# Optimization experiments

Measured on AMD Instinct MI355X. Metric: run time of the kernel, lower is better.

The kernel has to match this reference:

```python
import jax, jax.numpy as jnp
import numpy as np

B, C_IN, C_QKV, N = 8, 12, 36, 4096

def setup_inputs() -> dict:
    key = jax.random.key(0)
    ks = jax.random.split(key, 9)
    s_in = 1.0 / np.sqrt(C_IN)
    s_o = 1.0 / np.sqrt(C_QKV)
    return {
        "x": jax.random.normal(ks[0], (B, C_IN, N), dtype=jnp.float32),
        "wq": jax.random.uniform(ks[1], (C_QKV, C_IN), jnp.float32, -s_in, s_in),
        "bq": jax.random.uniform(ks[2], (C_QKV,), jnp.float32, -s_in, s_in),
        "wk": jax.random.uniform(ks[3], (C_QKV, C_IN), jnp.float32, -s_in, s_in),
        "bk": jax.random.uniform(ks[4], (C_QKV,), jnp.float32, -s_in, s_in),
        "wv": jax.random.uniform(ks[5], (C_QKV, C_IN), jnp.float32, -s_in, s_in),
        "bv": jax.random.uniform(ks[6], (C_QKV,), jnp.float32, -s_in, s_in),
        "wo": jax.random.uniform(ks[7], (C_IN, C_QKV), jnp.float32, -s_o, s_o),
        "bo": jax.random.uniform(ks[8], (C_IN,), jnp.float32, -s_o, s_o),
    }

def _conv1x1(w, b, x):
    # 1x1 Conv1d == channel-mixing matmul: [o,i] @ [b,i,n] -> [b,o,n]
    return jnp.einsum('oi,bin->bon', w, x) + b[None, :, None]

def reference(x, wq, bq, wk, bk, wv, bv, wo, bo):
    scale = 1.0 / jnp.sqrt(jnp.float32(x.shape[1]))  # 1/sqrt(12)
    q = _conv1x1(wq, bq, x)  # [B, 36, N]
    k = _conv1x1(wk, bk, x)
    v = _conv1x1(wv, bv, x)
    # inter = k^T @ q : scores[b,n,m] = sum_c k[b,c,n] * q[b,c,m]
    scores = jnp.einsum('bcn,bcm->bnm', k, q) * scale  # [B, N, N]
    weights = jax.nn.softmax(scores, axis=-1)
    attn = jnp.einsum('bcn,bnm->bcm', v, weights)  # v @ weights, [B, 36, N]
    return _conv1x1(wo, bo, attn)  # [B, 12, N]
```

## Files before the change

kernel.cpp:

```cpp
#include <hip/hip_runtime.h>
#include <hip/hip_bf16.h>
#include <math.h>

#define B 8
#define CIN 12
#define CQ 36
#define CP 48
#define N 4096
#define SCALE 0.28867513459481287f
#define LOG2E 1.4426950408889634f
#define ZSPLIT 8
#define NCHUNK (N / ZSPLIT)
#define NT (NCHUNK / 32)
#define MSPLIT 4

typedef __attribute__((ext_vector_type(4)))  short bf4_t;
typedef __attribute__((ext_vector_type(8)))  short bf8_t;
typedef __attribute__((ext_vector_type(16))) float f32x16;
typedef __attribute__((ext_vector_type(4)))  float f32x4;

__device__ __forceinline__ unsigned short f2bf(float x) {
  unsigned int u = __float_as_uint(x);
  u += 0x7FFFu + ((u >> 16) & 1u);
  return (unsigned short)(u >> 16);
}

#if __has_builtin(__builtin_amdgcn_cvt_pk_bf16_f32)
typedef __attribute__((ext_vector_type(2))) __bf16 bf16x2_t;
__device__ __forceinline__ unsigned pk2bf(float a, float b) {
  bf16x2_t v = __builtin_amdgcn_cvt_pk_bf16_f32(a, b);
  return __builtin_bit_cast(unsigned, v);
}
#else
__device__ __forceinline__ unsigned pk2bf(float a, float b) {
  return (__float_as_uint(a) >> 16) | (__float_as_uint(b) & 0xFFFF0000u);
}
#endif

__device__ __forceinline__ float bf2f(unsigned short u) {
  return __uint_as_float((unsigned)u << 16);
}

__device__ __forceinline__ float exp2fast(float x) {
#if __has_builtin(__builtin_amdgcn_exp2f)
  return __builtin_amdgcn_exp2f(x);
#else
  return exp2f(x);
#endif
}

__device__ __forceinline__ f32x4 mfma16(bf4_t a, bf4_t b, f32x4 c) {
#if __has_builtin(__builtin_amdgcn_mfma_f32_16x16x16bf16_1k)
  return __builtin_amdgcn_mfma_f32_16x16x16bf16_1k(a, b, c, 0, 0, 0);
#else
  bf8_t a8 = {a[0], a[1], a[2], a[3], 0, 0, 0, 0};
  bf8_t b8 = {b[0], b[1], b[2], b[3], 0, 0, 0, 0};
  return __builtin_amdgcn_mfma_f32_16x16x32_bf16(a8, b8, c, 0, 0, 0);
#endif
}

__device__ __forceinline__ bf8_t lds_bf8(const unsigned short* p) {
  uint2 a = *(const uint2*)p;
  uint2 b = *(const uint2*)(p + 4);
  uint4 r{a.x, a.y, b.x, b.y};
  return __builtin_bit_cast(bf8_t, r);
}
__device__ __forceinline__ void wlds16(unsigned short* p, uint4 v) {
  *(uint2*)p = uint2{v.x, v.y};
  *(uint2*)(p + 4) = uint2{v.z, v.w};
}

__global__ __launch_bounds__(256) void qkv_kernel(
    const float* __restrict__ x,
    const float* __restrict__ wq, const float* __restrict__ bq,
    const float* __restrict__ wk, const float* __restrict__ bk,
    const float* __restrict__ wv, const float* __restrict__ bv,
    unsigned short* __restrict__ qT, unsigned short* __restrict__ kT,
    unsigned short* __restrict__ vbf) {
  __shared__ float sw[CQ * CIN];
  __shared__ float sb[CQ];
  int z = blockIdx.y;
  const float* w  = (z == 0) ? wq : (z == 1) ? wk : wv;
  const float* bb = (z == 0) ? bq : (z == 1) ? bk : bv;
  float scale = (z == 1) ? SCALE * LOG2E : 1.0f;
  int tid = threadIdx.x;
  for (int e = tid; e < CQ * CIN; e += 256) sw[e] = w[e] * scale;
  if (tid < CQ) sb[tid] = bb[tid] * scale;
  __syncthreads();
  int gid = blockIdx.x * 256 + tid;
  int b = gid >> 12;
  int n = gid & (N - 1);
  float xv[CIN];
#pragma unroll
  for (int i = 0; i < CIN; ++i) xv[i] = x[(b * CIN + i) * N + n];
  if (z == 2) {
#pragma unroll
    for (int o = 0; o < CQ; ++o) {
      float a = sb[o];
#pragma unroll
      for (int i = 0; i < CIN; ++i) a += sw[o * CIN + i] * xv[i];
      vbf[((size_t)b * CP + o) * N + n] = f2bf(a);
    }
  } else {
    __attribute__((aligned(16))) unsigned row[CP / 2];
#pragma unroll
    for (int o = 0; o < CQ; o += 2) {
      float a0 = sb[o], a1 = sb[o + 1];
#pragma unroll
      for (int i = 0; i < CIN; ++i) {
        float xi = xv[i];
        a0 += sw[o * CIN + i] * xi;
        a1 += sw[(o + 1) * CIN + i] * xi;
      }
      row[o / 2] = (unsigned)f2bf(a0) | ((unsigned)f2bf(a1) << 16);
    }
    row[18] = (z == 0) ? 0x3F803F80u : 0u;
#pragma unroll
    for (int o = 19; o < CP / 2; ++o) row[o] = 0;
    unsigned short* dst = ((z == 0) ? qT : kT) + ((size_t)b * N + n) * CP;
#pragma unroll
    for (int i = 0; i < 6; ++i) *(uint4*)(dst + 8 * i) = *(const uint4*)&row[4 * i];
  }
}

__global__ __launch_bounds__(256) void stats_kernel(
    const unsigned short* __restrict__ qT, const unsigned short* __restrict__ kT,
    float* __restrict__ psum) {
  __shared__ float red[4][32];
  int tid = threadIdx.x, lane = tid & 63, wave = tid >> 6;
  int b = blockIdx.y, nblk = blockIdx.x, ms = blockIdx.z;
  int l31 = lane & 31, h = lane >> 5;
  const unsigned short* krow = kT + ((size_t)b * N + nblk * 32 + l31) * CP + h * 8;
  bf8_t a0 = *(const bf8_t*)(krow);
  bf8_t a1 = *(const bf8_t*)(krow + 16);
  bf8_t a2 = *(const bf8_t*)(krow + 32);
  float rs[16];
#pragma unroll
  for (int r = 0; r < 16; ++r) rs[r] = 0.f;
  const int MW = N / MSPLIT / 4;
  const unsigned short* qbase =
      qT + ((size_t)b * N + ms * (N / MSPLIT) + wave * MW + l31) * CP + h * 8;
#pragma unroll 2
  for (int t = 0; t < MW / 32; ++t) {
    const unsigned short* qrow2 = qbase + (size_t)t * 32 * CP;
    bf8_t b0 = *(const bf8_t*)(qrow2);
    bf8_t b1 = *(const bf8_t*)(qrow2 + 16);
    bf8_t b2 = *(const bf8_t*)(qrow2 + 32);
    f32x16 S;
#pragma unroll
    for (int r = 0; r < 16; ++r) S[r] = 0.f;
    S = __builtin_amdgcn_mfma_f32_32x32x16_bf16(a0, b0, S, 0, 0, 0);
    S = __builtin_amdgcn_mfma_f32_32x32x16_bf16(a1, b1, S, 0, 0, 0);
    S = __builtin_amdgcn_mfma_f32_32x32x16_bf16(a2, b2, S, 0, 0, 0);
#pragma unroll
    for (int r = 0; r < 16; ++r) rs[r] += exp2fast(S[r]);
  }
#pragma unroll
  for (int off = 16; off >= 1; off >>= 1)
#pragma unroll
    for (int r = 0; r < 16; ++r) rs[r] += __shfl_xor(rs[r], off, 32);
  if (l31 == 0) {
#pragma unroll
    for (int r = 0; r < 16; ++r) {
      int row = (r & 3) + 8 * (r >> 2) + 4 * h;
      red[wave][row] = rs[r];
    }
  }
  __syncthreads();
  if (tid < 32) {
    float s = red[0][tid] + red[1][tid] + red[2][tid] + red[3][tid];
    psum[((size_t)ms * B + b) * N + nblk * 32 + tid] = s;
  }
}

__global__ __launch_bounds__(256) void finalize_kernel(
    const float* __restrict__ psum, unsigned short* __restrict__ kT) {
  int gid = blockIdx.x * 256 + threadIdx.x;
  float L = 0.f;
#pragma unroll
  for (int ms = 0; ms < MSPLIT; ++ms) L += psum[(size_t)ms * B * N + gid];
  float t = -__log2f(L);
  unsigned short hi = f2bf(t);
  unsigned short lo = f2bf(t - bf2f(hi));
  size_t base = (size_t)gid * CP;
  kT[base + 36] = hi;
  kT[base + 37] = lo;
}

__global__ __launch_bounds__(256) void init_kernel(
    float* __restrict__ out, const float* __restrict__ bo) {
  int gid = blockIdx.x * 256 + threadIdx.x;
  int e4 = gid * 4;
  int i = (e4 >> 12) % CIN;
  float bv = bo[i];
  *(float4*)(out + e4) = float4{bv, bv, bv, bv};
}

__global__ __launch_bounds__(256, 5) void attn_kernel(
    const unsigned short* __restrict__ qT, const unsigned short* __restrict__ kT,
    const unsigned short* __restrict__ vbf, const float* __restrict__ wo,
    float* __restrict__ out) {
  __shared__ unsigned short kbuf[2][32 * 52];
  __shared__ unsigned short vbuf[2][48 * 36];
  __shared__ unsigned short plds[4][32 * 40];
  int tid = threadIdx.x, lane = tid & 63, wave = tid >> 6;
  int b = blockIdx.y, z = blockIdx.z, mblk = blockIdx.x;
  int l31 = lane & 31, h = lane >> 5, l15 = lane & 15, q4 = lane >> 4;
  int m0 = mblk * 128 + wave * 32;
  size_t bN = (size_t)b * N;
  bool isK0 = tid < 192;
  int r0row = isK0 ? (tid / 6) : ((tid - 192) >> 2);
  int r0c   = isK0 ? (tid % 6) : ((tid - 192) & 3);
  const unsigned short* s0 = isK0
      ? kT + (bN + z * NCHUNK + r0row) * CP + r0c * 8
      : vbf + ((size_t)b * CP + r0row) * N + z * NCHUNK + r0c * 8;
  int s0stride = isK0 ? 32 * CP : 32;
  unsigned short* dst0 = isK0 ? &kbuf[0][r0row * 52 + r0c * 8]
                              : &vbuf[0][r0row * 36 + r0c * 8];
  int dbs0 = isK0 ? 32 * 52 : 48 * 36;
  bool has1 = tid < 128;
  int r1row = (tid >> 2) + 16;
  int r1c = tid & 3;
  const unsigned short* s1 =
      vbf + ((size_t)b * CP + r1row) * N + z * NCHUNK + r1c * 8;
  unsigned short* dst1 = &vbuf[0][r1row * 36 + r1c * 8];
  const int dbs1 = 48 * 36;
  const unsigned short* qrow = qT + (bN + m0 + l31) * CP + h * 8;
  bf8_t qb0 = *(const bf8_t*)(qrow);
  bf8_t qb1 = *(const bf8_t*)(qrow + 16);
  bf8_t qb2 = *(const bf8_t*)(qrow + 32);
  bf4_t woa[3];
#pragma unroll
  for (int ct = 0; ct < 3; ++ct) {
    float4 w4 = {0.f, 0.f, 0.f, 0.f};
    int col = 16 * ct + q4 * 4;
    if (l15 < CIN && col < CQ) w4 = *(const float4*)(wo + l15 * CQ + col);
    woa[ct] = bf4_t{(short)f2bf(w4.x), (short)f2bf(w4.y),
                    (short)f2bf(w4.z), (short)f2bf(w4.w)};
  }
  f32x4 acc[3][2];
#pragma unroll
  for (int ct = 0; ct < 3; ++ct)
#pragma unroll
    for (int hm = 0; hm < 2; ++hm)
#pragma unroll
      for (int r = 0; r < 4; ++r) acc[ct][hm][r] = 0.f;
  unsigned short* pl = plds[wave];
  uint4 r0 = *(const uint4*)s0; s0 += s0stride;
  uint4 r1{0, 0, 0, 0};
  if (has1) { r1 = *(const uint4*)s1; s1 += 32; }
  wlds16(dst0, r0);
  if (has1) wlds16(dst1, r1);
  __syncthreads();
  for (int t = 0; t < NT; ++t) {
    int buf = t & 1;
    if (t + 1 < NT) {
      r0 = *(const uint4*)s0; s0 += s0stride;
      if (has1) { r1 = *(const uint4*)s1; s1 += 32; }
    }
    const unsigned short* kb = kbuf[buf];
    const unsigned short* vb = vbuf[buf];
    bf8_t a0 = lds_bf8(kb + l31 * 52 + h * 8);
    bf8_t a1 = lds_bf8(kb + l31 * 52 + h * 8 + 16);
    bf8_t a2 = lds_bf8(kb + l31 * 52 + h * 8 + 32);
    f32x16 S;
#pragma unroll
    for (int r = 0; r < 16; ++r) S[r] = 0.f;
    S = __builtin_amdgcn_mfma_f32_32x32x16_bf16(a0, qb0, S, 0, 0, 0);
    S = __builtin_amdgcn_mfma_f32_32x32x16_bf16(a1, qb1, S, 0, 0, 0);
    S = __builtin_amdgcn_mfma_f32_32x32x16_bf16(a2, qb2, S, 0, 0, 0);
#pragma unroll
    for (int qd = 0; qd < 4; ++qd) {
      uint2 pk;
      pk.x = pk2bf(exp2fast(S[4 * qd + 0]), exp2fast(S[4 * qd + 1]));
      pk.y = pk2bf(exp2fast(S[4 * qd + 2]), exp2fast(S[4 * qd + 3]));
      *(uint2*)&pl[l31 * 40 + 8 * qd + 4 * h] = pk;
    }
    bf8_t pb0 = *(const bf8_t*)&pl[l15 * 40 + q4 * 8];
    bf8_t pb1 = *(const bf8_t*)&pl[(16 + l15) * 40 + q4 * 8];
    bf8_t v0 = lds_bf8(vb + (0 * 16 + l15) * 36 + q4 * 8);
    bf8_t v1 = lds_bf8(vb + (1 * 16 + l15) * 36 + q4 * 8);
    bf8_t v2 = lds_bf8(vb + (2 * 16 + l15) * 36 + q4 * 8);
    acc[0][0] = __builtin_amdgcn_mfma_f32_16x16x32_bf16(v0, pb0, acc[0][0], 0, 0, 0);
    acc[0][1] = __builtin_amdgcn_mfma_f32_16x16x32_bf16(v0, pb1, acc[0][1], 0, 0, 0);
    acc[1][0] = __builtin_amdgcn_mfma_f32_16x16x32_bf16(v1, pb0, acc[1][0], 0, 0, 0);
    acc[1][1] = __builtin_amdgcn_mfma_f32_16x16x32_bf16(v1, pb1, acc[1][1], 0, 0, 0);
    acc[2][0] = __builtin_amdgcn_mfma_f32_16x16x32_bf16(v2, pb0, acc[2][0], 0, 0, 0);
    acc[2][1] = __builtin_amdgcn_mfma_f32_16x16x32_bf16(v2, pb1, acc[2][1], 0, 0, 0);
    if (t + 1 < NT) {
      int nb = buf ^ 1;
      wlds16(dst0 + nb * dbs0, r0);
      if (has1) wlds16(dst1 + nb * dbs1, r1);
    }
    __syncthreads();
  }
#pragma unroll
  for (int hm = 0; hm < 2; ++hm) {
    f32x4 po = {0.f, 0.f, 0.f, 0.f};
#pragma unroll
    for (int ct = 0; ct < 3; ++ct) {
      union { uint2 u; bf4_t v; } pb;
      pb.u.x = pk2bf(acc[ct][hm][0], acc[ct][hm][1]);
      pb.u.y = pk2bf(acc[ct][hm][2], acc[ct][hm][3]);
      po = mfma16(woa[ct], pb.v, po);
    }
    if (q4 < 3) {
      float* ob = out + ((size_t)b * CIN + q4 * 4) * N + m0 + hm * 16 + l15;
#pragma unroll
      for (int r = 0; r < 4; ++r) atomicAdd(ob + (size_t)r * N, po[r]);
    }
  }
}

extern "C" void kernel_launch(void* const* d_in, const int* in_sizes, int n_in,
                              void* d_out, int out_size, void* d_ws, size_t ws_size,
                              hipStream_t stream) {
  const float* x  = (const float*)d_in[0];
  const float* wq = (const float*)d_in[1];
  const float* bq = (const float*)d_in[2];
  const float* wk = (const float*)d_in[3];
  const float* bk = (const float*)d_in[4];
  const float* wv = (const float*)d_in[5];
  const float* bv = (const float*)d_in[6];
  const float* wo = (const float*)d_in[7];
  const float* bo = (const float*)d_in[8];
  float* out = (float*)d_out;

  char* ws = (char*)d_ws;
  unsigned short* qT  = (unsigned short*)ws;
  unsigned short* kT  = (unsigned short*)(ws + 3145728);
  unsigned short* vbf = (unsigned short*)(ws + 2 * 3145728);
  float* psum = (float*)(ws + 3 * 3145728);

  qkv_kernel<<<dim3(B * N / 256, 3), 256, 0, stream>>>(x, wq, bq, wk, bk, wv, bv,
                                                       qT, kT, vbf);
  stats_kernel<<<dim3(N / 32, B, MSPLIT), 256, 0, stream>>>(qT, kT, psum);
  finalize_kernel<<<B * N / 256, 256, 0, stream>>>(psum, kT);
  init_kernel<<<B * CIN * N / 1024, 256, 0, stream>>>(out, bo);
  attn_kernel<<<dim3(N / 128, B, ZSPLIT), 256, 0, stream>>>(qT, kT, vbf, wo, out);
}
```

Measured before the change: 151.4 us.

## Double per-wave tile in stats and attention kernels, merge finalize and init

The stats kernel now handles 64 key rows per block, with two accumulators sharing each loaded q fragment, and MSPLIT drops to 2. The attention kernel gives each wave 64 query columns instead of 32, so every K/V tile staged in LDS is reused twice and global traffic per unit of work halves. The finalize and init kernels are merged into one prep kernel, saving a launch. In exchange, register use and LDS per block go up, launch bounds fall from 5 to 3 blocks, and the grids shrink, which may leave parts of the GPU idle.

```diff
diff --git a/kernel.cpp b/kernel.cpp
--- a/kernel.cpp
+++ b/kernel.cpp
@@ -12,7 +12,7 @@
 #define ZSPLIT 8
 #define NCHUNK (N / ZSPLIT)
 #define NT (NCHUNK / 32)
-#define MSPLIT 4
+#define MSPLIT 2
 
 typedef __attribute__((ext_vector_type(4)))  short bf4_t;
 typedef __attribute__((ext_vector_type(8)))  short bf8_t;
@@ -126,87 +126,104 @@
 __global__ __launch_bounds__(256) void stats_kernel(
     const unsigned short* __restrict__ qT, const unsigned short* __restrict__ kT,
     float* __restrict__ psum) {
-  __shared__ float red[4][32];
+  __shared__ float red[4][64];
   int tid = threadIdx.x, lane = tid & 63, wave = tid >> 6;
   int b = blockIdx.y, nblk = blockIdx.x, ms = blockIdx.z;
   int l31 = lane & 31, h = lane >> 5;
-  const unsigned short* krow = kT + ((size_t)b * N + nblk * 32 + l31) * CP + h * 8;
-  bf8_t a0 = *(const bf8_t*)(krow);
-  bf8_t a1 = *(const bf8_t*)(krow + 16);
-  bf8_t a2 = *(const bf8_t*)(krow + 32);
-  float rs[16];
-#pragma unroll
-  for (int r = 0; r < 16; ++r) rs[r] = 0.f;
+  int n0 = nblk * 64;
+  size_t bN = (size_t)b * N;
+  const unsigned short* krow0 = kT + (bN + n0 + l31) * CP + h * 8;
+  const unsigned short* krow1 = krow0 + (size_t)32 * CP;
+  bf8_t a0 = *(const bf8_t*)(krow0);
+  bf8_t a1 = *(const bf8_t*)(krow0 + 16);
+  bf8_t a2 = *(const bf8_t*)(krow0 + 32);
+  bf8_t a3 = *(const bf8_t*)(krow1);
+  bf8_t a4 = *(const bf8_t*)(krow1 + 16);
+  bf8_t a5 = *(const bf8_t*)(krow1 + 32);
+  float rs0[16], rs1[16];
+#pragma unroll
+  for (int r = 0; r < 16; ++r) { rs0[r] = 0.f; rs1[r] = 0.f; }
   const int MW = N / MSPLIT / 4;
   const unsigned short* qbase =
-      qT + ((size_t)b * N + ms * (N / MSPLIT) + wave * MW + l31) * CP + h * 8;
+      qT + (bN + ms * (N / MSPLIT) + wave * MW + l31) * CP + h * 8;
 #pragma unroll 2
   for (int t = 0; t < MW / 32; ++t) {
     const unsigned short* qrow2 = qbase + (size_t)t * 32 * CP;
     bf8_t b0 = *(const bf8_t*)(qrow2);
     bf8_t b1 = *(const bf8_t*)(qrow2 + 16);
     bf8_t b2 = *(const bf8_t*)(qrow2 + 32);
-    f32x16 S;
-#pragma unroll
-    for (int r = 0; r < 16; ++r) S[r] = 0.f;
-    S = __builtin_amdgcn_mfma_f32_32x32x16_bf16(a0, b0, S, 0, 0, 0);
-    S = __builtin_amdgcn_mfma_f32_32x32x16_bf16(a1, b1, S, 0, 0, 0);
-    S = __builtin_amdgcn_mfma_f32_32x32x16_bf16(a2, b2, S, 0, 0, 0);
-#pragma unroll
-    for (int r = 0; r < 16; ++r) rs[r] += exp2fast(S[r]);
+    f32x16 S0, S1;
+#pragma unroll
+    for (int r = 0; r < 16; ++r) { S0[r] = 0.f; S1[r] = 0.f; }
+    S0 = __builtin_amdgcn_mfma_f32_32x32x16_bf16(a0, b0, S0, 0, 0, 0);
+    S0 = __builtin_amdgcn_mfma_f32_32x32x16_bf16(a1, b1, S0, 0, 0, 0);
+    S0 = __builtin_amdgcn_mfma_f32_32x32x16_bf16(a2, b2, S0, 0, 0, 0);
+    S1 = __builtin_amdgcn_mfma_f32_32x32x16_bf16(a3, b0, S1, 0, 0, 0);
+    S1 = __builtin_amdgcn_mfma_f32_32x32x16_bf16(a4, b1, S1, 0, 0, 0);
+    S1 = __builtin_amdgcn_mfma_f32_32x32x16_bf16(a5, b2, S1, 0, 0, 0);
+#pragma unroll
+    for (int r = 0; r < 16; ++r) {
+      rs0[r] += exp2fast(S0[r]);
+      rs1[r] += exp2fast(S1[r]);
+    }
   }
 #pragma unroll
   for (int off = 16; off >= 1; off >>= 1)
 #pragma unroll
-    for (int r = 0; r < 16; ++r) rs[r] += __shfl_xor(rs[r], off, 32);
+    for (int r = 0; r < 16; ++r) {
+      rs0[r] += __shfl_xor(rs0[r], off, 32);
+      rs1[r] += __shfl_xor(rs1[r], off, 32);
+    }
   if (l31 == 0) {
 #pragma unroll
     for (int r = 0; r < 16; ++r) {
       int row = (r & 3) + 8 * (r >> 2) + 4 * h;
-      red[wave][row] = rs[r];
+      red[wave][row] = rs0[r];
+      red[wave][32 + row] = rs1[r];
     }
   }
   __syncthreads();
-  if (tid < 32) {
+  if (tid < 64) {
     float s = red[0][tid] + red[1][tid] + red[2][tid] + red[3][tid];
-    psum[((size_t)ms * B + b) * N + nblk * 32 + tid] = s;
-  }
-}
-
-__global__ __launch_bounds__(256) void finalize_kernel(
-    const float* __restrict__ psum, unsigned short* __restrict__ kT) {
-  int gid = blockIdx.x * 256 + threadIdx.x;
-  float L = 0.f;
-#pragma unroll
-  for (int ms = 0; ms < MSPLIT; ++ms) L += psum[(size_t)ms * B * N + gid];
-  float t = -__log2f(L);
-  unsigned short hi = f2bf(t);
-  unsigned short lo = f2bf(t - bf2f(hi));
-  size_t base = (size_t)gid * CP;
-  kT[base + 36] = hi;
-  kT[base + 37] = lo;
-}
-
-__global__ __launch_bounds__(256) void init_kernel(
+    psum[((size_t)ms * B + b) * N + n0 + tid] = s;
+  }
+}
+
+__global__ __launch_bounds__(256) void prep_kernel(
+    const float* __restrict__ psum, unsigned short* __restrict__ kT,
     float* __restrict__ out, const float* __restrict__ bo) {
-  int gid = blockIdx.x * 256 + threadIdx.x;
-  int e4 = gid * 4;
-  int i = (e4 >> 12) % CIN;
-  float bv = bo[i];
-  *(float4*)(out + e4) = float4{bv, bv, bv, bv};
-}
-
-__global__ __launch_bounds__(256, 5) void attn_kernel(
+  int bx = blockIdx.x, tid = threadIdx.x;
+  if (bx < B * N / 256) {
+    int gid = bx * 256 + tid;
+    float L = 0.f;
+#pragma unroll
+    for (int ms = 0; ms < MSPLIT; ++ms) L += psum[(size_t)ms * B * N + gid];
+    float t = -__log2f(L);
+    unsigned short hi = f2bf(t);
+    unsigned short lo = f2bf(t - bf2f(hi));
+    size_t base = (size_t)gid * CP;
+    kT[base + 36] = hi;
+    kT[base + 37] = lo;
+  } else {
+    int gid = (bx - B * N / 256) * 256 + tid;
+    int e4 = gid * 4;
+    int i = (e4 >> 12) % CIN;
+    float bv = bo[i];
+    *(float4*)(out + e4) = float4{bv, bv, bv, bv};
+  }
+}
+
+__global__ __launch_bounds__(256, 3) void attn_kernel(
     const unsigned short* __restrict__ qT, const unsigned short* __restrict__ kT,
     const unsigned short* __restrict__ vbf, const float* __restrict__ wo,
     float* __restrict__ out) {
   __shared__ unsigned short kbuf[2][32 * 52];
   __shared__ unsigned short vbuf[2][48 * 36];
-  __shared__ unsigned short plds[4][32 * 40];
+  __shared__ unsigned short plds[4][2][32 * 40];
   int tid = threadIdx.x, lane = tid & 63, wave = tid >> 6;
   int b = blockIdx.y, z = blockIdx.z, mblk = blockIdx.x;
   int l31 = lane & 31, h = lane >> 5, l15 = lane & 15, q4 = lane >> 4;
-  int m0 = mblk * 128 + wave * 32;
+  int m0 = mblk * 256 + wave * 64;
   size_t bN = (size_t)b * N;
   bool isK0 = tid < 192;
   int r0row = isK0 ? (tid / 6) : ((tid - 192) >> 2);
@@ -225,10 +242,14 @@
       vbf + ((size_t)b * CP + r1row) * N + z * NCHUNK + r1c * 8;
   unsigned short* dst1 = &vbuf[0][r1row * 36 + r1c * 8];
   const int dbs1 = 48 * 36;
-  const unsigned short* qrow = qT + (bN + m0 + l31) * CP + h * 8;
-  bf8_t qb0 = *(const bf8_t*)(qrow);
-  bf8_t qb1 = *(const bf8_t*)(qrow + 16);
-  bf8_t qb2 = *(const bf8_t*)(qrow + 32);
+  bf8_t qb[2][3];
+#pragma unroll
+  for (int mt = 0; mt < 2; ++mt) {
+    const unsigned short* qrow = qT + (bN + m0 + mt * 32 + l31) * CP + h * 8;
+    qb[mt][0] = *(const bf8_t*)(qrow);
+    qb[mt][1] = *(const bf8_t*)(qrow + 16);
+    qb[mt][2] = *(const bf8_t*)(qrow + 32);
+  }
   bf4_t woa[3];
 #pragma unroll
   for (int ct = 0; ct < 3; ++ct) {
@@ -238,14 +259,15 @@
     woa[ct] = bf4_t{(short)f2bf(w4.x), (short)f2bf(w4.y),
                     (short)f2bf(w4.z), (short)f2bf(w4.w)};
   }
-  f32x4 acc[3][2];
-#pragma unroll
-  for (int ct = 0; ct < 3; ++ct)
-#pragma unroll
-    for (int hm = 0; hm < 2; ++hm)
-#pragma unroll
-      for (int r = 0; r < 4; ++r) acc[ct][hm][r] = 0.f;
-  unsigned short* pl = plds[wave];
+  f32x4 acc[2][3][2];
+#pragma unroll
+  for (int mt = 0; mt < 2; ++mt)
+#pragma unroll
+    for (int ct = 0; ct < 3; ++ct)
+#pragma unroll
+      for (int hm = 0; hm < 2; ++hm)
+#pragma unroll
+        for (int r = 0; r < 4; ++r) acc[mt][ct][hm][r] = 0.f;
   uint4 r0 = *(const uint4*)s0; s0 += s0stride;
   uint4 r1{0, 0, 0, 0};
   if (has1) { r1 = *(const uint4*)s1; s1 += 32; }
@@ -263,30 +285,38 @@
     bf8_t a0 = lds_bf8(kb + l31 * 52 + h * 8);
     bf8_t a1 = lds_bf8(kb + l31 * 52 + h * 8 + 16);
     bf8_t a2 = lds_bf8(kb + l31 * 52 + h * 8 + 32);
-    f32x16 S;
-#pragma unroll
-    for (int r = 0; r < 16; ++r) S[r] = 0.f;
-    S = __builtin_amdgcn_mfma_f32_32x32x16_bf16(a0, qb0, S, 0, 0, 0);
-    S = __builtin_amdgcn_mfma_f32_32x32x16_bf16(a1, qb1, S, 0, 0, 0);
-    S = __builtin_amdgcn_mfma_f32_32x32x16_bf16(a2, qb2, S, 0, 0, 0);
-#pragma unroll
-    for (int qd = 0; qd < 4; ++qd) {
-      uint2 pk;
-      pk.x = pk2bf(exp2fast(S[4 * qd + 0]), exp2fast(S[4 * qd + 1]));
-      pk.y = pk2bf(exp2fast(S[4 * qd + 2]), exp2fast(S[4 * qd + 3]));
-      *(uint2*)&pl[l31 * 40 + 8 * qd + 4 * h] = pk;
-    }
-    bf8_t pb0 = *(const bf8_t*)&pl[l15 * 40 + q4 * 8];
-    bf8_t pb1 = *(const bf8_t*)&pl[(16 + l15) * 40 + q4 * 8];
+#pragma unroll
+    for (int mt = 0; mt < 2; ++mt) {
+      f32x16 S;
+#pragma unroll
+      for (int r = 0; r < 16; ++r) S[r] = 0.f;
+      S = __builtin_amdgcn_mfma_f32_32x32x16_bf16(a0, qb[mt][0], S, 0, 0, 0);
+      S = __builtin_amdgcn_mfma_f32_32x32x16_bf16(a1, qb[mt][1], S, 0, 0, 0);
+      S = __builtin_amdgcn_mfma_f32_32x32x16_bf16(a2, qb[mt][2], S, 0, 0, 0);
+      unsigned short* pl = plds[wave][mt];
+#pragma unroll
+      for (int qd = 0; qd < 4; ++qd) {
+        uint2 pk;
+        pk.x = pk2bf(exp2fast(S[4 * qd + 0]), exp2fast(S[4 * qd + 1]));
+        pk.y = pk2bf(exp2fast(S[4 * qd + 2]), exp2fast(S[4 * qd + 3]));
+        *(uint2*)&pl[l31 * 40 + 8 * qd + 4 * h] = pk;
+      }
+    }
     bf8_t v0 = lds_bf8(vb + (0 * 16 + l15) * 36 + q4 * 8);
     bf8_t v1 = lds_bf8(vb + (1 * 16 + l15) * 36 + q4 * 8);
     bf8_t v2 = lds_bf8(vb + (2 * 16 + l15) * 36 + q4 * 8);
-    acc[0][0] = __builtin_amdgcn_mfma_f32_16x16x32_bf16(v0, pb0, acc[0][0], 0, 0, 0);
-    acc[0][1] = __builtin_amdgcn_mfma_f32_16x16x32_bf16(v0, pb1, acc[0][1], 0, 0, 0);
-    acc[1][0] = __builtin_amdgcn_mfma_f32_16x16x32_bf16(v1, pb0, acc[1][0], 0, 0, 0);
-    acc[1][1] = __builtin_amdgcn_mfma_f32_16x16x32_bf16(v1, pb1, acc[1][1], 0, 0, 0);
-    acc[2][0] = __builtin_amdgcn_mfma_f32_16x16x32_bf16(v2, pb0, acc[2][0], 0, 0, 0);
-    acc[2][1] = __builtin_amdgcn_mfma_f32_16x16x32_bf16(v2, pb1, acc[2][1], 0, 0, 0);
+#pragma unroll
+    for (int mt = 0; mt < 2; ++mt) {
+      const unsigned short* pl = plds[wave][mt];
+      bf8_t pb0 = *(const bf8_t*)&pl[l15 * 40 + q4 * 8];
+      bf8_t pb1 = *(const bf8_t*)&pl[(16 + l15) * 40 + q4 * 8];
+      acc[mt][0][0] = __builtin_amdgcn_mfma_f32_16x16x32_bf16(v0, pb0, acc[mt][0][0], 0, 0, 0);
+      acc[mt][0][1] = __builtin_amdgcn_mfma_f32_16x16x32_bf16(v0, pb1, acc[mt][0][1], 0, 0, 0);
+      acc[mt][1][0] = __builtin_amdgcn_mfma_f32_16x16x32_bf16(v1, pb0, acc[mt][1][0], 0, 0, 0);
+      acc[mt][1][1] = __builtin_amdgcn_mfma_f32_16x16x32_bf16(v1, pb1, acc[mt][1][1], 0, 0, 0);
+      acc[mt][2][0] = __builtin_amdgcn_mfma_f32_16x16x32_bf16(v2, pb0, acc[mt][2][0], 0, 0, 0);
+      acc[mt][2][1] = __builtin_amdgcn_mfma_f32_16x16x32_bf16(v2, pb1, acc[mt][2][1], 0, 0, 0);
+    }
     if (t + 1 < NT) {
       int nb = buf ^ 1;
       wlds16(dst0 + nb * dbs0, r0);
@@ -295,21 +325,23 @@
     __syncthreads();
   }
 #pragma unroll
-  for (int hm = 0; hm < 2; ++hm) {
-    f32x4 po = {0.f, 0.f, 0.f, 0.f};
-#pragma unroll
-    for (int ct = 0; ct < 3; ++ct) {
-      union { uint2 u; bf4_t v; } pb;
-      pb.u.x = pk2bf(acc[ct][hm][0], acc[ct][hm][1]);
-      pb.u.y = pk2bf(acc[ct][hm][2], acc[ct][hm][3]);
-      po = mfma16(woa[ct], pb.v, po);
-    }
-    if (q4 < 3) {
-      float* ob = out + ((size_t)b * CIN + q4 * 4) * N + m0 + hm * 16 + l15;
-#pragma unroll
-      for (int r = 0; r < 4; ++r) atomicAdd(ob + (size_t)r * N, po[r]);
-    }
-  }
+  for (int mt = 0; mt < 2; ++mt)
+#pragma unroll
+    for (int hm = 0; hm < 2; ++hm) {
+      f32x4 po = {0.f, 0.f, 0.f, 0.f};
+#pragma unroll
+      for (int ct = 0; ct < 3; ++ct) {
+        union { uint2 u; bf4_t v; } pb;
+        pb.u.x = pk2bf(acc[mt][ct][hm][0], acc[mt][ct][hm][1]);
+        pb.u.y = pk2bf(acc[mt][ct][hm][2], acc[mt][ct][hm][3]);
+        po = mfma16(woa[ct], pb.v, po);
+      }
+      if (q4 < 3) {
+        float* ob = out + ((size_t)b * CIN + q4 * 4) * N + m0 + mt * 32 + hm * 16 + l15;
+#pragma unroll
+        for (int r = 0; r < 4; ++r) atomicAdd(ob + (size_t)r * N, po[r]);
+      }
+    }
 }
 
 extern "C" void kernel_launch(void* const* d_in, const int* in_sizes, int n_in,
@@ -334,8 +366,7 @@
 
   qkv_kernel<<<dim3(B * N / 256, 3), 256, 0, stream>>>(x, wq, bq, wk, bk, wv, bv,
                                                        qT, kT, vbf);
-  stats_kernel<<<dim3(N / 32, B, MSPLIT), 256, 0, stream>>>(qT, kT, psum);
-  finalize_kernel<<<B * N / 256, 256, 0, stream>>>(psum, kT);
-  init_kernel<<<B * CIN * N / 1024, 256, 0, stream>>>(out, bo);
-  attn_kernel<<<dim3(N / 128, B, ZSPLIT), 256, 0, stream>>>(qT, kT, vbf, wo, out);
-}
+  stats_kernel<<<dim3(N / 64, B, MSPLIT), 256, 0, stream>>>(qT, kT, psum);
+  prep_kernel<<<B * N / 256 + B * CIN * N / 1024, 256, 0, stream>>>(psum, kT, out, bo);
+  attn_kernel<<<dim3(N / 256, B, ZSPLIT), 256, 0, stream>>>(qT, kT, vbf, wo, out);
+}
```

Result: faster. 135.9 us (-10.3%).
